# Optimization experiments

Measured on AMD Instinct MI355X. Metric: run time of the kernel, lower is better.

Reference implementation:

```python
import jax, jax.numpy as jnp
import numpy as np

L = 65536   # sequence length (keys/values)
D = 512     # embed dim (hardcoded in source)
H = 4       # heads
HD = 128    # head dim

def _ln(x, g, b):
    m = jnp.mean(x, -1, keepdims=True)
    v = jnp.var(x, -1, keepdims=True)
    return (x - m) * jax.lax.rsqrt(v + 1e-5) * g + b

def setup_inputs() -> dict:
    key = jax.random.key(0)
    ks = jax.random.split(key, 6)
    s = 0.02
    return {
        "x": jax.random.normal(ks[0], (L, D), jnp.float32),
        "w_in": jax.random.normal(ks[1], (3 * D, D), jnp.float32) * s,
        "b_in": jnp.zeros((3 * D,), jnp.float32),
        "w_out": jax.random.normal(ks[2], (D, D), jnp.float32) * s,
        "b_out": jnp.zeros((D,), jnp.float32),
        "w1": jax.random.normal(ks[3], (D, D), jnp.float32) * s,
        "b1": jnp.zeros((D,), jnp.float32),
        "w2": jax.random.normal(ks[4], (D, D), jnp.float32) * s,
        "b2": jnp.zeros((D,), jnp.float32),
        "g1": jnp.ones((D,), jnp.float32),
        "be1": jnp.zeros((D,), jnp.float32),
        "g2": jnp.ones((D,), jnp.float32),
        "be2": jnp.zeros((D,), jnp.float32),
    }

def reference(x, w_in, b_in, w_out, b_out, w1, b1, w2, b2, g1, be1, g2, be2):
    xn = _ln(x, g1, be1)                               # [L, D]
    q = xn[:1] @ w_in[:D].T + b_in[:D]                 # [1, D] single-row query
    k = xn @ w_in[D:2 * D].T + b_in[D:2 * D]           # [L, D]
    v = xn @ w_in[2 * D:].T + b_in[2 * D:]             # [L, D]
    qh = q.reshape(H, HD)                              # [H, HD]
    kh = k.reshape(L, H, HD)
    vh = v.reshape(L, H, HD)
    scores = jnp.einsum('hd,lhd->hl', qh, kh) * (1.0 / np.sqrt(HD))  # [H, L]
    attn = jax.nn.softmax(scores, axis=-1)
    o = jnp.einsum('hl,lhd->hd', attn, vh).reshape(1, D)             # [1, D]
    o = o @ w_out.T + b_out
    y = x[:1] + o                                      # residual keeps only row 0
    yn = _ln(y, g2, be2)
    h = jax.nn.relu(yn @ w1.T + b1)
    return y + h @ w2.T + b2                           # [1, D]
```

## Files before the change

### kernel.cpp

```cpp
#include <hip/hip_runtime.h>
#include <math.h>

#define DD 512


__device__ __forceinline__ float dot4(float4 a, float4 b) {
    return a.x * b.x + a.y * b.y + a.z * b.z + a.w * b.w;
}
__device__ __forceinline__ float wred(float v) {
#pragma unroll
    for (int m = 32; m; m >>= 1) v += __shfl_xor(v, m, 64);
    return v;
}
__device__ __forceinline__ float4 f4fma(float4 acc, float s, float4 v) {
    acc.x += s * v.x; acc.y += s * v.y; acc.z += s * v.z; acc.w += s * v.w;
    return acc;
}
__device__ __forceinline__ float4 f4add(float4 a, float4 b) {
    a.x += b.x; a.y += b.y; a.z += b.z; a.w += b.w; return a;
}
__device__ __forceinline__ float4 f4muls(float4 a, float4 g, float s) {
    a.x *= g.x * s; a.y *= g.y * s; a.z *= g.z * s; a.w *= g.w * s; return a;
}
__device__ __forceinline__ float hsum4(float4 a) { return a.x + a.y + a.z + a.w; }
__device__ __forceinline__ float4 lnrm4(float4 v, float m, float r, float4 g, float4 b) {
    float4 o;
    o.x = (v.x - m) * r * g.x + b.x; o.y = (v.y - m) * r * g.y + b.y;
    o.z = (v.z - m) * r * g.z + b.z; o.w = (v.w - m) * r * g.w + b.w;
    return o;
}
__device__ __forceinline__ float4 caff4(float4 c, float inv, float w2t, float4 g, float4 b) {
    float4 o;
    o.x = g.x * (c.x * inv - w2t) + b.x; o.y = g.y * (c.y * inv - w2t) + b.y;
    o.z = g.z * (c.z * inv - w2t) + b.z; o.w = g.w * (c.w * inv - w2t) + b.w;
    return o;
}

__global__ __launch_bounds__(512) void kA(const float* __restrict__ x,
                                          const float* __restrict__ w_in,
                                          const float* __restrict__ b_in,
                                          const float* __restrict__ g1,
                                          const float* __restrict__ be1,
                                          float* __restrict__ ws) {
    __shared__ float qh[32];
    int bi = blockIdx.x, tid = threadIdx.x, lane = tid & 63, w = tid >> 6;
    int h = bi >> 2, c = bi & 3;
    {
        float4 z = make_float4(0.f, 0.f, 0.f, 0.f);
        ((float4*)(ws + 8448))[bi * 512 + tid] = z;
        if (bi == 0 && tid < 128) ws[8192 + tid] = 0.f;
    }
    const float4* x4 = (const float4*)x;
    float4 a = x4[lane], b = x4[64 + lane];
    float ps = wred(hsum4(a) + hsum4(b));
    float pss = wred(dot4(a, a) + dot4(b, b));
    float m = ps * (1.f / 512.f);
    float r = rsqrtf(pss * (1.f / 512.f) - m * m + 1e-5f);
    const float4* g4 = (const float4*)g1;
    const float4* bb4 = (const float4*)be1;
    float4 xna = lnrm4(a, m, r, g4[lane], bb4[lane]);
    float4 xnb = lnrm4(b, m, r, g4[64 + lane], bb4[64 + lane]);
    int j0 = h * 128 + c * 32;
    const float4* wr = (const float4*)(w_in + (size_t)(j0 + w * 4) * DD);
    for (int i = 0; i < 4; ++i) {
        float acc = wred(dot4(wr[i * 128 + lane], xna) + dot4(wr[i * 128 + 64 + lane], xnb));
        if (lane == 0) qh[w * 4 + i] = acc + b_in[j0 + w * 4 + i];
    }
    __syncthreads();
    const float* wk = w_in + (size_t)(DD + j0) * DD + tid;
    float acc = 0.f;
#pragma unroll
    for (int d = 0; d < 32; ++d) acc += qh[d] * wk[(size_t)d * DD];
    ws[c * 2048 + h * 512 + tid] = acc;
}

__global__ __launch_bounds__(512) void kB(const float* __restrict__ x,
                                          const float* __restrict__ g1,
                                          float* __restrict__ ws) {
    __shared__ float lds[16384];
    int tid = threadIdx.x, lane = tid & 63, w = tid >> 6;
    const float4* p4 = (const float4*)ws;
    const float4* g4 = (const float4*)g1;
    const float scale = 0.088388347648318447f;
    float4 ga = g4[lane], gb = g4[64 + lane];
    float4 qa[4], qb[4];
    float qs[4];
#pragma unroll
    for (int h = 0; h < 4; ++h) {
        float4 sa = f4add(f4add(p4[h * 128 + lane], p4[512 + h * 128 + lane]),
                          f4add(p4[1024 + h * 128 + lane], p4[1536 + h * 128 + lane]));
        float4 sb = f4add(f4add(p4[h * 128 + 64 + lane], p4[512 + h * 128 + 64 + lane]),
                          f4add(p4[1024 + h * 128 + 64 + lane], p4[1536 + h * 128 + 64 + lane]));
        qa[h] = f4muls(sa, ga, scale);
        qb[h] = f4muls(sb, gb, scale);
        qs[h] = wred(hsum4(qa[h]) + hsum4(qb[h]));
    }
    float sm[4], w2a[4];
    float4 Wa[4], Wb[4];
#pragma unroll
    for (int h = 0; h < 4; ++h) {
        sm[h] = 0.f; w2a[h] = 0.f;
        Wa[h] = make_float4(0.f, 0.f, 0.f, 0.f);
        Wb[h] = make_float4(0.f, 0.f, 0.f, 0.f);
    }
    size_t row0 = ((size_t)blockIdx.x * 8 + w) * 16;
    const float4* xb = (const float4*)x + row0 * 128;
    float4 nxa = xb[lane], nxc = xb[64 + lane];
    for (int r = 0; r < 16; ++r) {
        float4 xa = nxa, xc = nxc;
        if (r < 15) { nxa = xb[(r + 1) * 128 + lane]; nxc = xb[(r + 1) * 128 + 64 + lane]; }
        float ps = hsum4(xa) + hsum4(xc);
        float pss = dot4(xa, xa) + dot4(xc, xc);
        float p0 = dot4(xa, qa[0]) + dot4(xc, qb[0]);
        float p1 = dot4(xa, qa[1]) + dot4(xc, qb[1]);
        float p2 = dot4(xa, qa[2]) + dot4(xc, qb[2]);
        float p3 = dot4(xa, qa[3]) + dot4(xc, qb[3]);
        ps = wred(ps); pss = wred(pss);
        p0 = wred(p0); p1 = wred(p1); p2 = wred(p2); p3 = wred(p3);
        float m = ps * (1.f / 512.f);
        float rr = rsqrtf(pss * (1.f / 512.f) - m * m + 1e-5f);
        float rm = rr * m;
        float pd[4] = {p0, p1, p2, p3};
#pragma unroll
        for (int h = 0; h < 4; ++h) {
            float s = rr * pd[h] - rm * qs[h];
            float p = __expf(s);
            sm[h] += p;
            w2a[h] += p * rm;
            float pr = p * rr;
            Wa[h] = f4fma(Wa[h], pr, xa);
            Wb[h] = f4fma(Wb[h], pr, xc);
        }
    }
    int copy = blockIdx.x & 15;
    if (lane == 0) {
#pragma unroll
        for (int h = 0; h < 4; ++h) {
            lds[w * 4 + h] = sm[h];
            lds[32 + w * 4 + h] = w2a[h];
        }
    }
    __syncthreads();
    if (tid < 8) {
        int h = tid & 3;
        float a = 0.f;
        if (tid < 4) {
            for (int ww = 0; ww < 8; ++ww) a += lds[ww * 4 + h];
            atomicAdd(&ws[8192 + copy * 4 + h], a);
        } else {
            for (int ww = 0; ww < 8; ++ww) a += lds[32 + ww * 4 + h];
            atomicAdd(&ws[8256 + copy * 4 + h], a);
        }
    }
    __syncthreads();
    float4* lw4 = (float4*)(lds + w * 2048);
#pragma unroll
    for (int h = 0; h < 4; ++h) {
        lw4[h * 128 + lane] = Wa[h];
        lw4[h * 128 + 64 + lane] = Wb[h];
    }
    __syncthreads();
    float* cdst = ws + 8448 + (size_t)copy * 2048;
    for (int i = tid; i < 2048; i += 512) {
        float a = lds[i] + lds[2048 + i] + lds[4096 + i] + lds[6144 + i] +
                  lds[8192 + i] + lds[10240 + i] + lds[12288 + i] + lds[14336 + i];
        atomicAdd(cdst + i, a);
    }
}

__global__ __launch_bounds__(256) void kD1(const float* __restrict__ w_in,
                                           const float* __restrict__ b_in,
                                           const float* __restrict__ g1,
                                           const float* __restrict__ be1,
                                           float* __restrict__ ws) {
    int tid = threadIdx.x, lane = tid & 63, w = tid >> 6;
    int j = blockIdx.x * 4 + w;
    int h = j >> 7;
    float smg = 0.f, w2g = 0.f;
#pragma unroll
    for (int c = 0; c < 16; ++c) {
        smg += ws[8192 + c * 4 + h];
        w2g += ws[8256 + c * 4 + h];
    }
    float inv = 1.f / smg, w2t = w2g * inv;
    float4 cra = make_float4(0.f, 0.f, 0.f, 0.f), crb = cra;
#pragma unroll
    for (int c = 0; c < 16; ++c) {
        const float4* cr = (const float4*)(ws + 8448 + c * 2048 + h * 512);
        cra = f4add(cra, cr[lane]);
        crb = f4add(crb, cr[64 + lane]);
    }
    const float4* g14 = (const float4*)g1;
    const float4* be14 = (const float4*)be1;
    float4 ca = caff4(cra, inv, w2t, g14[lane], be14[lane]);
    float4 cb = caff4(crb, inv, w2t, g14[64 + lane], be14[64 + lane]);
    const float4* wr = (const float4*)(w_in + (size_t)(2 * DD + j) * DD);
    float acc = wred(dot4(wr[lane], ca) + dot4(wr[64 + lane], cb));
    if (lane == 0) ws[41216 + j] = acc + b_in[2 * DD + j];
}

__global__ __launch_bounds__(256) void kD2(const float* __restrict__ x,
                                           const float* __restrict__ w_out,
                                           const float* __restrict__ b_out,
                                           float* __restrict__ ws) {
    int lane = threadIdx.x & 63;
    int j = blockIdx.x * 4 + (threadIdx.x >> 6);
    const float4* wr = (const float4*)(w_out + (size_t)j * DD);
    const float4* o4 = (const float4*)(ws + 41216);
    float acc = wred(dot4(wr[lane], o4[lane]) + dot4(wr[64 + lane], o4[64 + lane]));
    if (lane == 0) ws[41728 + j] = x[j] + acc + b_out[j];
}

__global__ __launch_bounds__(256) void kD3(const float* __restrict__ w1,
                                           const float* __restrict__ b1,
                                           const float* __restrict__ g2,
                                           const float* __restrict__ be2,
                                           float* __restrict__ ws) {
    int lane = threadIdx.x & 63;
    int j = blockIdx.x * 4 + (threadIdx.x >> 6);
    const float4* y4 = (const float4*)(ws + 41728);
    float4 ya = y4[lane], yb = y4[64 + lane];
    float ps = wred(hsum4(ya) + hsum4(yb));
    float pss = wred(dot4(ya, ya) + dot4(yb, yb));
    float m2 = ps * (1.f / 512.f);
    float r2 = rsqrtf(pss * (1.f / 512.f) - m2 * m2 + 1e-5f);
    const float4* g4 = (const float4*)g2;
    const float4* b4 = (const float4*)be2;
    float4 yna = lnrm4(ya, m2, r2, g4[lane], b4[lane]);
    float4 ynb = lnrm4(yb, m2, r2, g4[64 + lane], b4[64 + lane]);
    const float4* wr = (const float4*)(w1 + (size_t)j * DD);
    float acc = wred(dot4(wr[lane], yna) + dot4(wr[64 + lane], ynb));
    if (lane == 0) ws[42240 + j] = fmaxf(acc + b1[j], 0.f);
}

__global__ __launch_bounds__(256) void kD4(const float* __restrict__ w2,
                                           const float* __restrict__ b2,
                                           const float* __restrict__ ws,
                                           float* __restrict__ out) {
    int lane = threadIdx.x & 63;
    int j = blockIdx.x * 4 + (threadIdx.x >> 6);
    const float4* h4 = (const float4*)(ws + 42240);
    const float4* wr = (const float4*)(w2 + (size_t)j * DD);
    float acc = wred(dot4(wr[lane], h4[lane]) + dot4(wr[64 + lane], h4[64 + lane]));
    if (lane == 0) out[j] = ws[41728 + j] + acc + b2[j];
}

extern "C" void kernel_launch(void* const* d_in, const int* in_sizes, int n_in,
                              void* d_out, int out_size, void* d_ws, size_t ws_size,
                              hipStream_t stream) {
    (void)in_sizes; (void)n_in; (void)out_size; (void)ws_size;
    const float* x = (const float*)d_in[0];
    const float* w_in = (const float*)d_in[1];
    const float* b_in = (const float*)d_in[2];
    const float* w_out = (const float*)d_in[3];
    const float* b_out = (const float*)d_in[4];
    const float* w1 = (const float*)d_in[5];
    const float* b1 = (const float*)d_in[6];
    const float* w2 = (const float*)d_in[7];
    const float* b2 = (const float*)d_in[8];
    const float* g1 = (const float*)d_in[9];
    const float* be1 = (const float*)d_in[10];
    const float* g2 = (const float*)d_in[11];
    const float* be2 = (const float*)d_in[12];
    float* ws = (float*)d_ws;
    float* out = (float*)d_out;

    hipLaunchKernelGGL(kA, dim3(16), dim3(512), 0, stream, x, w_in, b_in, g1, be1, ws);
    hipLaunchKernelGGL(kB, dim3(512), dim3(512), 0, stream, x, g1, ws);
    hipLaunchKernelGGL(kD1, dim3(128), dim3(256), 0, stream, w_in, b_in, g1, be1, ws);
    hipLaunchKernelGGL(kD2, dim3(128), dim3(256), 0, stream, x, w_out, b_out, ws);
    hipLaunchKernelGGL(kD3, dim3(128), dim3(256), 0, stream, w1, b1, g2, be2, ws);
    hipLaunchKernelGGL(kD4, dim3(128), dim3(256), 0, stream, w2, b2, ws, out);
}
```

Baseline: 236.6 us.

## Fuse tail matvec kernels into one cooperative kernel and widen kA split

Merges the four small tail kernels (V projection, output projection, LN2+FFN1, FFN2) into one cooperative kernel that uses grid-wide syncs in place of kernel boundaries. This removes three launch gaps for tiny, latency-bound work. It also splits the kA query/key-projection work across 32 blocks of 16 rows instead of 16 blocks of 32, moves the workspace offsets, and makes kB sum eight partials. Grid syncs have their own cost, and cooperative launch may carry extra overhead.

```diff
diff --git a/kernel.cpp b/kernel.cpp
--- a/kernel.cpp
+++ b/kernel.cpp
@@ -1,5 +1,8 @@
 #include <hip/hip_runtime.h>
+#include <hip/hip_cooperative_groups.h>
 #include <math.h>
+
+namespace cg = cooperative_groups;
 
 #define DD 512
 
@@ -42,14 +45,12 @@
                                           const float* __restrict__ g1,
                                           const float* __restrict__ be1,
                                           float* __restrict__ ws) {
-    __shared__ float qh[32];
+    __shared__ float qh[16];
     int bi = blockIdx.x, tid = threadIdx.x, lane = tid & 63, w = tid >> 6;
-    int h = bi >> 2, c = bi & 3;
-    {
-        float4 z = make_float4(0.f, 0.f, 0.f, 0.f);
-        ((float4*)(ws + 8448))[bi * 512 + tid] = z;
-        if (bi == 0 && tid < 128) ws[8192 + tid] = 0.f;
-    }
+    int h = bi >> 3, c = bi & 7;
+    ws[16512 + bi * 1024 + tid] = 0.f;
+    ws[16512 + bi * 1024 + 512 + tid] = 0.f;
+    if (bi == 0 && tid < 128) ws[16384 + tid] = 0.f;
     const float4* x4 = (const float4*)x;
     float4 a = x4[lane], b = x4[64 + lane];
     float ps = wred(hsum4(a) + hsum4(b));
@@ -60,17 +61,17 @@
     const float4* bb4 = (const float4*)be1;
     float4 xna = lnrm4(a, m, r, g4[lane], bb4[lane]);
     float4 xnb = lnrm4(b, m, r, g4[64 + lane], bb4[64 + lane]);
-    int j0 = h * 128 + c * 32;
-    const float4* wr = (const float4*)(w_in + (size_t)(j0 + w * 4) * DD);
-    for (int i = 0; i < 4; ++i) {
+    int j0 = h * 128 + c * 16;
+    const float4* wr = (const float4*)(w_in + (size_t)(j0 + w * 2) * DD);
+    for (int i = 0; i < 2; ++i) {
         float acc = wred(dot4(wr[i * 128 + lane], xna) + dot4(wr[i * 128 + 64 + lane], xnb));
-        if (lane == 0) qh[w * 4 + i] = acc + b_in[j0 + w * 4 + i];
+        if (lane == 0) qh[w * 2 + i] = acc + b_in[j0 + w * 2 + i];
     }
     __syncthreads();
     const float* wk = w_in + (size_t)(DD + j0) * DD + tid;
     float acc = 0.f;
 #pragma unroll
-    for (int d = 0; d < 32; ++d) acc += qh[d] * wk[(size_t)d * DD];
+    for (int d = 0; d < 16; ++d) acc += qh[d] * wk[(size_t)d * DD];
     ws[c * 2048 + h * 512 + tid] = acc;
 }
 
@@ -87,10 +88,12 @@
     float qs[4];
 #pragma unroll
     for (int h = 0; h < 4; ++h) {
-        float4 sa = f4add(f4add(p4[h * 128 + lane], p4[512 + h * 128 + lane]),
-                          f4add(p4[1024 + h * 128 + lane], p4[1536 + h * 128 + lane]));
-        float4 sb = f4add(f4add(p4[h * 128 + 64 + lane], p4[512 + h * 128 + 64 + lane]),
-                          f4add(p4[1024 + h * 128 + 64 + lane], p4[1536 + h * 128 + 64 + lane]));
+        float4 sa = make_float4(0.f, 0.f, 0.f, 0.f), sb = sa;
+#pragma unroll
+        for (int c = 0; c < 8; ++c) {
+            sa = f4add(sa, p4[c * 512 + h * 128 + lane]);
+            sb = f4add(sb, p4[c * 512 + h * 128 + 64 + lane]);
+        }
         qa[h] = f4muls(sa, ga, scale);
         qb[h] = f4muls(sb, gb, scale);
         qs[h] = wred(hsum4(qa[h]) + hsum4(qb[h]));
@@ -146,10 +149,10 @@
         float a = 0.f;
         if (tid < 4) {
             for (int ww = 0; ww < 8; ++ww) a += lds[ww * 4 + h];
-            atomicAdd(&ws[8192 + copy * 4 + h], a);
+            atomicAdd(&ws[16384 + copy * 4 + h], a);
         } else {
             for (int ww = 0; ww < 8; ++ww) a += lds[32 + ww * 4 + h];
-            atomicAdd(&ws[8256 + copy * 4 + h], a);
+            atomicAdd(&ws[16448 + copy * 4 + h], a);
         }
     }
     __syncthreads();
@@ -160,7 +163,7 @@
         lw4[h * 128 + 64 + lane] = Wb[h];
     }
     __syncthreads();
-    float* cdst = ws + 8448 + (size_t)copy * 2048;
+    float* cdst = ws + 16512 + (size_t)copy * 2048;
     for (int i = tid; i < 2048; i += 512) {
         float a = lds[i] + lds[2048 + i] + lds[4096 + i] + lds[6144 + i] +
                   lds[8192 + i] + lds[10240 + i] + lds[12288 + i] + lds[14336 + i];
@@ -168,81 +171,82 @@
     }
 }
 
-__global__ __launch_bounds__(256) void kD1(const float* __restrict__ w_in,
-                                           const float* __restrict__ b_in,
-                                           const float* __restrict__ g1,
-                                           const float* __restrict__ be1,
-                                           float* __restrict__ ws) {
+__global__ __launch_bounds__(256) void kD(const float* __restrict__ x,
+                                          const float* __restrict__ w_in,
+                                          const float* __restrict__ b_in,
+                                          const float* __restrict__ w_out,
+                                          const float* __restrict__ b_out,
+                                          const float* __restrict__ w1,
+                                          const float* __restrict__ b1,
+                                          const float* __restrict__ w2,
+                                          const float* __restrict__ b2,
+                                          const float* __restrict__ g1,
+                                          const float* __restrict__ be1,
+                                          const float* __restrict__ g2,
+                                          const float* __restrict__ be2,
+                                          float* __restrict__ ws,
+                                          float* __restrict__ out) {
+    cg::grid_group grid = cg::this_grid();
     int tid = threadIdx.x, lane = tid & 63, w = tid >> 6;
     int j = blockIdx.x * 4 + w;
-    int h = j >> 7;
-    float smg = 0.f, w2g = 0.f;
-#pragma unroll
-    for (int c = 0; c < 16; ++c) {
-        smg += ws[8192 + c * 4 + h];
-        w2g += ws[8256 + c * 4 + h];
-    }
-    float inv = 1.f / smg, w2t = w2g * inv;
-    float4 cra = make_float4(0.f, 0.f, 0.f, 0.f), crb = cra;
-#pragma unroll
-    for (int c = 0; c < 16; ++c) {
-        const float4* cr = (const float4*)(ws + 8448 + c * 2048 + h * 512);
-        cra = f4add(cra, cr[lane]);
-        crb = f4add(crb, cr[64 + lane]);
-    }
-    const float4* g14 = (const float4*)g1;
-    const float4* be14 = (const float4*)be1;
-    float4 ca = caff4(cra, inv, w2t, g14[lane], be14[lane]);
-    float4 cb = caff4(crb, inv, w2t, g14[64 + lane], be14[64 + lane]);
-    const float4* wr = (const float4*)(w_in + (size_t)(2 * DD + j) * DD);
-    float acc = wred(dot4(wr[lane], ca) + dot4(wr[64 + lane], cb));
-    if (lane == 0) ws[41216 + j] = acc + b_in[2 * DD + j];
-}
-
-__global__ __launch_bounds__(256) void kD2(const float* __restrict__ x,
-                                           const float* __restrict__ w_out,
-                                           const float* __restrict__ b_out,
-                                           float* __restrict__ ws) {
-    int lane = threadIdx.x & 63;
-    int j = blockIdx.x * 4 + (threadIdx.x >> 6);
-    const float4* wr = (const float4*)(w_out + (size_t)j * DD);
-    const float4* o4 = (const float4*)(ws + 41216);
-    float acc = wred(dot4(wr[lane], o4[lane]) + dot4(wr[64 + lane], o4[64 + lane]));
-    if (lane == 0) ws[41728 + j] = x[j] + acc + b_out[j];
-}
-
-__global__ __launch_bounds__(256) void kD3(const float* __restrict__ w1,
-                                           const float* __restrict__ b1,
-                                           const float* __restrict__ g2,
-                                           const float* __restrict__ be2,
-                                           float* __restrict__ ws) {
-    int lane = threadIdx.x & 63;
-    int j = blockIdx.x * 4 + (threadIdx.x >> 6);
-    const float4* y4 = (const float4*)(ws + 41728);
-    float4 ya = y4[lane], yb = y4[64 + lane];
-    float ps = wred(hsum4(ya) + hsum4(yb));
-    float pss = wred(dot4(ya, ya) + dot4(yb, yb));
-    float m2 = ps * (1.f / 512.f);
-    float r2 = rsqrtf(pss * (1.f / 512.f) - m2 * m2 + 1e-5f);
-    const float4* g4 = (const float4*)g2;
-    const float4* b4 = (const float4*)be2;
-    float4 yna = lnrm4(ya, m2, r2, g4[lane], b4[lane]);
-    float4 ynb = lnrm4(yb, m2, r2, g4[64 + lane], b4[64 + lane]);
-    const float4* wr = (const float4*)(w1 + (size_t)j * DD);
-    float acc = wred(dot4(wr[lane], yna) + dot4(wr[64 + lane], ynb));
-    if (lane == 0) ws[42240 + j] = fmaxf(acc + b1[j], 0.f);
-}
-
-__global__ __launch_bounds__(256) void kD4(const float* __restrict__ w2,
-                                           const float* __restrict__ b2,
-                                           const float* __restrict__ ws,
-                                           float* __restrict__ out) {
-    int lane = threadIdx.x & 63;
-    int j = blockIdx.x * 4 + (threadIdx.x >> 6);
-    const float4* h4 = (const float4*)(ws + 42240);
-    const float4* wr = (const float4*)(w2 + (size_t)j * DD);
-    float acc = wred(dot4(wr[lane], h4[lane]) + dot4(wr[64 + lane], h4[64 + lane]));
-    if (lane == 0) out[j] = ws[41728 + j] + acc + b2[j];
+
+    {
+        int h = j >> 7;
+        float smg = 0.f, w2g = 0.f;
+#pragma unroll
+        for (int c = 0; c < 16; ++c) {
+            smg += ws[16384 + c * 4 + h];
+            w2g += ws[16448 + c * 4 + h];
+        }
+        float inv = 1.f / smg, w2t = w2g * inv;
+        float4 cra = make_float4(0.f, 0.f, 0.f, 0.f), crb = cra;
+#pragma unroll
+        for (int c = 0; c < 16; ++c) {
+            const float4* cr = (const float4*)(ws + 16512 + c * 2048 + h * 512);
+            cra = f4add(cra, cr[lane]);
+            crb = f4add(crb, cr[64 + lane]);
+        }
+        const float4* g14 = (const float4*)g1;
+        const float4* be14 = (const float4*)be1;
+        float4 ca = caff4(cra, inv, w2t, g14[lane], be14[lane]);
+        float4 cb = caff4(crb, inv, w2t, g14[64 + lane], be14[64 + lane]);
+        const float4* wr = (const float4*)(w_in + (size_t)(2 * DD + j) * DD);
+        float acc = wred(dot4(wr[lane], ca) + dot4(wr[64 + lane], cb));
+        if (lane == 0) ws[49280 + j] = acc + b_in[2 * DD + j];
+    }
+    grid.sync();
+
+    {
+        const float4* wr = (const float4*)(w_out + (size_t)j * DD);
+        const float4* o4 = (const float4*)(ws + 49280);
+        float acc = wred(dot4(wr[lane], o4[lane]) + dot4(wr[64 + lane], o4[64 + lane]));
+        if (lane == 0) ws[49792 + j] = x[j] + acc + b_out[j];
+    }
+    grid.sync();
+
+    {
+        const float4* y4 = (const float4*)(ws + 49792);
+        float4 ya = y4[lane], yb = y4[64 + lane];
+        float ps = wred(hsum4(ya) + hsum4(yb));
+        float pss = wred(dot4(ya, ya) + dot4(yb, yb));
+        float m2 = ps * (1.f / 512.f);
+        float r2 = rsqrtf(pss * (1.f / 512.f) - m2 * m2 + 1e-5f);
+        const float4* g4 = (const float4*)g2;
+        const float4* b4 = (const float4*)be2;
+        float4 yna = lnrm4(ya, m2, r2, g4[lane], b4[lane]);
+        float4 ynb = lnrm4(yb, m2, r2, g4[64 + lane], b4[64 + lane]);
+        const float4* wr = (const float4*)(w1 + (size_t)j * DD);
+        float acc = wred(dot4(wr[lane], yna) + dot4(wr[64 + lane], ynb));
+        if (lane == 0) ws[50304 + j] = fmaxf(acc + b1[j], 0.f);
+    }
+    grid.sync();
+
+    {
+        const float4* h4 = (const float4*)(ws + 50304);
+        const float4* wr = (const float4*)(w2 + (size_t)j * DD);
+        float acc = wred(dot4(wr[lane], h4[lane]) + dot4(wr[64 + lane], h4[64 + lane]));
+        if (lane == 0) out[j] = ws[49792 + j] + acc + b2[j];
+    }
 }
 
 extern "C" void kernel_launch(void* const* d_in, const int* in_sizes, int n_in,
@@ -265,10 +269,14 @@
     float* ws = (float*)d_ws;
     float* out = (float*)d_out;
 
-    hipLaunchKernelGGL(kA, dim3(16), dim3(512), 0, stream, x, w_in, b_in, g1, be1, ws);
+    hipLaunchKernelGGL(kA, dim3(32), dim3(512), 0, stream, x, w_in, b_in, g1, be1, ws);
     hipLaunchKernelGGL(kB, dim3(512), dim3(512), 0, stream, x, g1, ws);
-    hipLaunchKernelGGL(kD1, dim3(128), dim3(256), 0, stream, w_in, b_in, g1, be1, ws);
-    hipLaunchKernelGGL(kD2, dim3(128), dim3(256), 0, stream, x, w_out, b_out, ws);
-    hipLaunchKernelGGL(kD3, dim3(128), dim3(256), 0, stream, w1, b1, g2, be2, ws);
-    hipLaunchKernelGGL(kD4, dim3(128), dim3(256), 0, stream, w2, b2, ws, out);
-}
+
+    void* args[] = {
+        (void*)&x, (void*)&w_in, (void*)&b_in, (void*)&w_out, (void*)&b_out,
+        (void*)&w1, (void*)&b1, (void*)&w2, (void*)&b2,
+        (void*)&g1, (void*)&be1, (void*)&g2, (void*)&be2,
+        (void*)&ws, (void*)&out
+    };
+    hipLaunchCooperativeKernel((const void*)kD, dim3(128), dim3(256), args, 0, stream);
+}
```

Result: slower. 304.8 us (+28.8%).
